# Performance work log

Measured on AMD Instinct MI355X. Metric: run time of the kernel, lower is better.

Reference implementation:

```python
import jax, jax.numpy as jnp
import numpy as np

R = 4e-4
NON = 0.05


def _conv1x1(x, w, b):
    # 1x1 conv, NCHW: [B,C,H,W] x [D,C] -> [B,D,H,W]
    return jnp.einsum('bchw,dc->bdhw', x, w) + b[None, :, None, None]


def _branch(x, si_w, si_b, fi_w, fi_b, gi_w, gi_b, fsg_w, fsg_b):
    B, C, W, H = x.shape
    N = W * H
    s = _conv1x1(x, si_w, si_b).reshape(B, C, N)
    f = _conv1x1(x, fi_w, fi_b).reshape(B, C, N)
    g = _conv1x1(x, gi_w, gi_b).reshape(B, C, N)
    # F = s^T @ f : [B, N, N]
    Fm = jnp.einsum('bcn,bcm->bnm', s, f)
    # original normalizes by global (per-sample) max & sum over the whole
    # [N,N] matrix -> a softmax over the flattened matrix. The exp-sum is
    # always > 0 (exp(0)=1 at the max), so the conditional is always taken.
    NF = jax.nn.softmax(Fm.reshape(B, N * N), axis=-1).reshape(B, N, N)
    gn = jnp.einsum('bcn,bnm->bcm', g, NF).reshape(B, C, W, H)
    fsg = _conv1x1(gn, fsg_w, fsg_b)
    # spatial mean pooling of residual sum -> [B, C]
    return (x + fsg).sum(axis=(2, 3)) / N


def setup_inputs() -> dict:
    key = jax.random.key(0)
    ks = jax.random.split(key, 10)
    B, C, W, H = 4, 64, 64, 64
    sc = 1.0 / np.sqrt(C)
    d = {
        'student': jax.random.normal(ks[0], (B, C, W, H), jnp.float32),
        'teacher': jax.random.normal(ks[1], (B, C, W, H), jnp.float32),
    }
    for i, nm in enumerate(['si', 'fi', 'gi', 'fsg']):
        d[nm + '_w'] = jax.random.normal(ks[2 + 2 * i], (C, C), jnp.float32) * sc
        d[nm + '_b'] = jax.random.normal(ks[3 + 2 * i], (C,), jnp.float32) * sc
    return d


def reference(student, teacher, si_w, si_b, fi_w, fi_b, gi_w, gi_b, fsg_w, fsg_b):
    out_stu = _branch(student, si_w, si_b, fi_w, fi_b, gi_w, gi_b, fsg_w, fsg_b)
    out_tea = _branch(teacher, si_w, si_b, fi_w, fi_b, gi_w, gi_b, fsg_w, fsg_b)
    B = student.shape[0]
    n_levels = 1  # len(student) in the original list-of-features API
    lnon = jnp.sum((out_stu - out_tea) ** 2)  # MSELoss(reduction='sum')
    non_loss = NON * R * lnon / B / n_levels
    return non_loss * B, jax.lax.stop_gradient(non_loss)[None]
```

## Files before the change

### kernel.cpp

```cpp
#include <hip/hip_runtime.h>
#include <hip/hip_bf16.h>
#include <stdint.h>

typedef __bf16 bf16x8 __attribute__((ext_vector_type(8)));
typedef float  f32x4  __attribute__((ext_vector_type(4)));

union U16x8 { bf16x8 v; unsigned short s[8]; uint4 q; };

#define SCH_SCALE 12102203.0f
#define SCH_BIAS  1064986823.0f

__device__ inline unsigned short f2bf(float f) {
  union { float f; unsigned int u; } x; x.f = f;
  unsigned int r = x.u + 0x7FFFu + ((x.u >> 16) & 1u);
  return (unsigned short)(r >> 16);
}
__device__ inline float bf2f(unsigned short u) {
  union { unsigned int u; float f; } x; x.u = ((unsigned int)u) << 16; return x.f;
}

__global__ __launch_bounds__(256) void k_proj(
    const float* __restrict__ stu, const float* __restrict__ tea,
    const float* __restrict__ si_w, const float* __restrict__ fi_w, const float* __restrict__ gi_w,
    const float* __restrict__ si_b, const float* __restrict__ fi_b, const float* __restrict__ gi_b,
    unsigned short* __restrict__ sT, unsigned short* __restrict__ fT, unsigned short* __restrict__ gT,
    float* __restrict__ Sxp) {
  int bid = blockIdx.x;
  int br_ba = bid & 7;
  int nt = bid >> 3;
  int br = br_ba >> 2, ba = br_ba & 3;
  const float* x = (br ? tea : stu) + (size_t)ba * 64 * 4096;
  int t = threadIdx.x;
  int wid = t >> 6, l = t & 63, g = l >> 4, lr = l & 15;
  int n0 = nt * 128 + wid * 32;

  U16x8 afr[2][2];
  float sx[2][8];
  #pragma unroll
  for (int kh = 0; kh < 2; ++kh)
    #pragma unroll
    for (int j = 0; j < 8; ++j) sx[kh][j] = 0.f;

  #pragma unroll
  for (int rf = 0; rf < 2; ++rf) {
    int n = n0 + rf * 16 + lr;
    #pragma unroll
    for (int kh = 0; kh < 2; ++kh) {
      #pragma unroll
      for (int j = 0; j < 8; ++j) {
        int c = kh * 32 + g * 8 + j;
        float v = x[(size_t)c * 4096 + n];
        afr[rf][kh].s[j] = f2bf(v);
        sx[kh][j] += v;
      }
    }
  }
  #pragma unroll
  for (int kh = 0; kh < 2; ++kh)
    #pragma unroll
    for (int j = 0; j < 8; ++j) {
      float v = sx[kh][j];
      v += __shfl_xor(v, 1); v += __shfl_xor(v, 2);
      v += __shfl_xor(v, 4); v += __shfl_xor(v, 8);
      sx[kh][j] = v;
    }
  __shared__ float sxl[4][64];
  if (lr == 0) {
    #pragma unroll
    for (int kh = 0; kh < 2; ++kh)
      #pragma unroll
      for (int j = 0; j < 8; ++j)
        sxl[wid][kh * 32 + g * 8 + j] = sx[kh][j];
  }
  __syncthreads();
  if (t < 64)
    Sxp[bid * 64 + t] = (sxl[0][t] + sxl[1][t]) + (sxl[2][t] + sxl[3][t]);

  size_t obase = (size_t)br_ba * 4096 * 64;
  auto proj_one = [&](const float* w, const float* bias, float scale,
                      unsigned short* op, int frag) {
    U16x8 bfr[4][2];
    #pragma unroll
    for (int cf = 0; cf < 4; ++cf) {
      int d = cf * 16 + lr;
      #pragma unroll
      for (int kh = 0; kh < 2; ++kh) {
        const float* wr = w + d * 64 + kh * 32 + g * 8;
        float4 w0 = *(const float4*)(wr);
        float4 w1 = *(const float4*)(wr + 4);
        bfr[cf][kh].s[0] = f2bf(w0.x * scale); bfr[cf][kh].s[1] = f2bf(w0.y * scale);
        bfr[cf][kh].s[2] = f2bf(w0.z * scale); bfr[cf][kh].s[3] = f2bf(w0.w * scale);
        bfr[cf][kh].s[4] = f2bf(w1.x * scale); bfr[cf][kh].s[5] = f2bf(w1.y * scale);
        bfr[cf][kh].s[6] = f2bf(w1.z * scale); bfr[cf][kh].s[7] = f2bf(w1.w * scale);
      }
    }
    f32x4 acc[2][4];
    #pragma unroll
    for (int rf = 0; rf < 2; ++rf)
      #pragma unroll
      for (int cf = 0; cf < 4; ++cf)
        acc[rf][cf] = (f32x4){0.f, 0.f, 0.f, 0.f};
    #pragma unroll
    for (int kh = 0; kh < 2; ++kh)
      #pragma unroll
      for (int rf = 0; rf < 2; ++rf)
        #pragma unroll
        for (int cf = 0; cf < 4; ++cf)
          acc[rf][cf] = __builtin_amdgcn_mfma_f32_16x16x32_bf16(
              afr[rf][kh].v, bfr[cf][kh].v, acc[rf][cf], 0, 0, 0);
    #pragma unroll
    for (int cf = 0; cf < 4; ++cf) {
      float bias_v = bias[cf * 16 + lr] * scale;
      int c = cf * 16 + lr;
      #pragma unroll
      for (int rf = 0; rf < 2; ++rf) {
        int sl = nt * 8 + wid * 2 + rf;
        #pragma unroll
        for (int r = 0; r < 4; ++r) {
          int n = n0 + rf * 16 + g * 4 + r;
          unsigned short val = f2bf(acc[rf][cf][r] + bias_v);
          if (frag) {
            size_t idx = ((size_t)(sl * 2 + (c >> 5)) * 64
                          + (g * 4 + r) + 16 * ((c >> 3) & 3)) * 8 + (c & 7);
            op[idx] = val;
          } else {
            op[(size_t)n * 64 + c] = val;
          }
        }
      }
    }
  };
  proj_one(si_w, si_b, SCH_SCALE, sT + obase, 1);
  proj_one(fi_w, fi_b, 1.0f, fT + obase, 1);
  proj_one(gi_w, gi_b, 1.0f, gT + obase, 0);
}

__global__ __launch_bounds__(256) void k_scores(
    const unsigned short* __restrict__ sT, const unsigned short* __restrict__ fT,
    float* __restrict__ stats_w) {
  int bid = blockIdx.x;
  int br_ba = bid & 7;
  int rest = bid >> 3;
  int cg = rest & 15;
  int rg = rest >> 4;
  int t = threadIdx.x;
  int wid = t >> 6, l = t & 63, g = l >> 4, lr = l & 15;

  const bf16x8* sfr = (const bf16x8*)sT + (size_t)br_ba * 32768;
  const bf16x8* ffr = (const bf16x8*)fT + (size_t)br_ba * 32768;

  const bf16x8* sp = sfr + (size_t)(cg * 16 + wid * 4) * 128 + l;
  bf16x8 b0k0 = sp[0];   bf16x8 b0k1 = sp[64];
  bf16x8 b1k0 = sp[128]; bf16x8 b1k1 = sp[192];
  bf16x8 b2k0 = sp[256]; bf16x8 b2k1 = sp[320];
  bf16x8 b3k0 = sp[384]; bf16x8 b3k1 = sp[448];

  const bf16x8* fp = ffr + (size_t)(rg * 32) * 128 + l;

  const f32x4 biasv = (f32x4){SCH_BIAS, SCH_BIAS, SCH_BIAS, SCH_BIAS};
  f32x4 S0 = (f32x4){0.f,0.f,0.f,0.f}, S1 = S0, S2 = S0, S3 = S0;

  bf16x8 cur0 = fp[0], cur1 = fp[64];

  #pragma unroll 2
  for (int k = 0; k < 32; ++k) {
    bf16x8 nxt0, nxt1;
    if (k < 31) {
      nxt0 = fp[(size_t)(k + 1) * 128];
      nxt1 = fp[(size_t)(k + 1) * 128 + 64];
    }
    f32x4 a0 = __builtin_amdgcn_mfma_f32_16x16x32_bf16(cur0, b0k0, biasv, 0,0,0);
    f32x4 a1 = __builtin_amdgcn_mfma_f32_16x16x32_bf16(cur0, b1k0, biasv, 0,0,0);
    f32x4 a2 = __builtin_amdgcn_mfma_f32_16x16x32_bf16(cur0, b2k0, biasv, 0,0,0);
    f32x4 a3 = __builtin_amdgcn_mfma_f32_16x16x32_bf16(cur0, b3k0, biasv, 0,0,0);
    a0 = __builtin_amdgcn_mfma_f32_16x16x32_bf16(cur1, b0k1, a0, 0,0,0);
    a1 = __builtin_amdgcn_mfma_f32_16x16x32_bf16(cur1, b1k1, a1, 0,0,0);
    a2 = __builtin_amdgcn_mfma_f32_16x16x32_bf16(cur1, b2k1, a2, 0,0,0);
    a3 = __builtin_amdgcn_mfma_f32_16x16x32_bf16(cur1, b3k1, a3, 0,0,0);
    #pragma unroll
    for (int r = 0; r < 4; ++r) {
      S0[r] += __uint_as_float((unsigned int)a0[r]);
      S1[r] += __uint_as_float((unsigned int)a1[r]);
      S2[r] += __uint_as_float((unsigned int)a2[r]);
      S3[r] += __uint_as_float((unsigned int)a3[r]);
    }
    cur0 = nxt0; cur1 = nxt1;
  }

  float w0 = (S0[0] + S0[1]) + (S0[2] + S0[3]);
  float w1 = (S1[0] + S1[1]) + (S1[2] + S1[3]);
  float w2 = (S2[0] + S2[1]) + (S2[2] + S2[3]);
  float w3 = (S3[0] + S3[1]) + (S3[2] + S3[3]);
  w0 += __shfl_xor(w0, 16); w0 += __shfl_xor(w0, 32);
  w1 += __shfl_xor(w1, 16); w1 += __shfl_xor(w1, 32);
  w2 += __shfl_xor(w2, 16); w2 += __shfl_xor(w2, 32);
  w3 += __shfl_xor(w3, 16); w3 += __shfl_xor(w3, 32);
  if (g == 0) {
    size_t cb = (size_t)br_ba * 4096 + cg * 256 + wid * 64 + lr;
    stats_w[(cb +  0) * 8 + rg] = w0;
    stats_w[(cb + 16) * 8 + rg] = w1;
    stats_w[(cb + 32) * 8 + rg] = w2;
    stats_w[(cb + 48) * 8 + rg] = w3;
  }
}

__global__ __launch_bounds__(256) void k_gbar(const unsigned short* __restrict__ gT,
                                              const float* __restrict__ stats_w,
                                              float* __restrict__ gbar_part,
                                              float* __restrict__ zpart) {
  int bid = blockIdx.x;
  int br_ba = bid & 7;
  int seg = bid >> 3;
  int t = threadIdx.x;
  int n0 = seg * 64;

  __shared__ float wlds[64];
  if (t < 64) {
    const float4* p = (const float4*)(stats_w + ((size_t)br_ba * 4096 + n0 + t) * 8);
    float4 a = p[0], b = p[1];
    float w = ((a.x + a.y) + (a.z + a.w)) + ((b.x + b.y) + (b.z + b.w));
    float zsum = w;
    zsum += __shfl_xor(zsum, 1);  zsum += __shfl_xor(zsum, 2);
    zsum += __shfl_xor(zsum, 4);  zsum += __shfl_xor(zsum, 8);
    zsum += __shfl_xor(zsum, 16); zsum += __shfl_xor(zsum, 32);
    if (t == 0) zpart[br_ba * 64 + seg] = zsum;
    wlds[t] = w;
  }
  __syncthreads();

  int c = t & 63, part = t >> 6;
  const unsigned short* gp = gT + ((size_t)br_ba * 4096 + n0) * 64;
  float acc = 0.f;
  #pragma unroll 4
  for (int r = 0; r < 16; ++r) {
    int k = part * 16 + r;
    acc += wlds[k] * bf2f(gp[(size_t)k * 64 + c]);
  }
  __shared__ float red[256];
  red[t] = acc; __syncthreads();
  if (t < 64)
    gbar_part[(size_t)(br_ba * 64 + seg) * 64 + c] =
        red[t] + red[t + 64] + red[t + 128] + red[t + 192];
}

__global__ __launch_bounds__(256) void k_loss(const float* __restrict__ Sxp,
                                              const float* __restrict__ gbar_part,
                                              const float* __restrict__ zpart,
                                              const float* __restrict__ fsg_w,
                                              float* __restrict__ out) {
  int t = threadIdx.x;
  int ba = t >> 6, d = t & 63;
  __shared__ float zsh[8];
  if (t < 8) {
    float z = 0.f;
    for (int s2 = 0; s2 < 64; ++s2) z += zpart[t * 64 + s2];
    zsh[t] = z;
  }
  float gs = 0.f, gt_ = 0.f;
  for (int seg = 0; seg < 64; ++seg) {
    gs  += gbar_part[(size_t)((0 + ba) * 64 + seg) * 64 + d];
    gt_ += gbar_part[(size_t)((4 + ba) * 64 + seg) * 64 + d];
  }
  float sxs = 0.f, sxt = 0.f;
  for (int nt = 0; nt < 32; ++nt) {
    sxs += Sxp[(nt * 8 + 0 + ba) * 64 + d];
    sxt += Sxp[(nt * 8 + 4 + ba) * 64 + d];
  }
  __syncthreads();
  __shared__ float gdiff[4][64];
  gdiff[ba][d] = gs / zsh[ba] - gt_ / zsh[4 + ba];
  __syncthreads();
  float dot = 0.f;
  for (int c = 0; c < 64; ++c) dot += fsg_w[d * 64 + c] * gdiff[ba][c];
  float diff = ((sxs - sxt) + dot) * (1.0f / 4096.0f);
  __shared__ float red[256];
  red[t] = diff * diff; __syncthreads();
  for (int s = 128; s > 0; s >>= 1) { if (t < s) red[t] += red[t + s]; __syncthreads(); }
  if (t == 0) {
    float lnon = red[0];
    out[0] = 2e-5f * lnon;
    out[1] = 2e-5f * lnon * 0.25f;
  }
}

extern "C" void kernel_launch(void* const* d_in, const int* in_sizes, int n_in,
                              void* d_out, int out_size, void* d_ws, size_t ws_size,
                              hipStream_t stream) {
  const float* stu   = (const float*)d_in[0];
  const float* tea   = (const float*)d_in[1];
  const float* si_w  = (const float*)d_in[2];
  const float* si_b  = (const float*)d_in[3];
  const float* fi_w  = (const float*)d_in[4];
  const float* fi_b  = (const float*)d_in[5];
  const float* gi_w  = (const float*)d_in[6];
  const float* gi_b  = (const float*)d_in[7];
  const float* fsg_w = (const float*)d_in[8];

  char* ws = (char*)d_ws;
  size_t off = 0;
  auto alloc = [&](size_t bytes) -> void* {
    void* p = ws + off;
    off = (off + bytes + 255) & ~(size_t)255;
    return p;
  };
  unsigned short* sT  = (unsigned short*)alloc((size_t)8 * 4096 * 64 * 2);
  unsigned short* fT  = (unsigned short*)alloc((size_t)8 * 4096 * 64 * 2);
  unsigned short* gT  = (unsigned short*)alloc((size_t)8 * 4096 * 64 * 2);
  float* stats_w      = (float*)alloc((size_t)8 * 4096 * 8 * 4);
  float* Sxp          = (float*)alloc((size_t)256 * 64 * 4);
  float* zpart        = (float*)alloc(512 * 4);
  float* gbar_part    = (float*)alloc((size_t)8 * 64 * 64 * 4);
  float* out          = (float*)d_out;

  k_proj<<<256, 256, 0, stream>>>(stu, tea, si_w, fi_w, gi_w, si_b, fi_b, gi_b, sT, fT, gT, Sxp);
  k_scores<<<1024, 256, 0, stream>>>(sT, fT, stats_w);
  k_gbar<<<512, 256, 0, stream>>>(gT, stats_w, gbar_part, zpart);
  k_loss<<<1, 256, 0, stream>>>(Sxp, gbar_part, zpart, fsg_w, out);
}
```

Measured before the change: 46.13 us.

## Fuse gbar and loss kernels via last-block atomic ticket reduction

Merges the gbar partial-sum kernel and the single-block loss kernel into one launch: each block atomically takes a ticket and the last block to finish does the final reduction and loss. The grid drops from 512 to 128 blocks, each covering 256 positions instead of 64, so there are fewer partials to reduce. The counter is zeroed inside k_proj. This removes one kernel launch and its gap, but lowers parallelism in the gbar phase and adds threadfence/atomic overhead.

Result: slower. 52.62 us (+14.1%).

```diff
diff --git a/kernel.cpp b/kernel.cpp
--- a/kernel.cpp
+++ b/kernel.cpp
@@ -24,8 +24,9 @@
     const float* __restrict__ si_w, const float* __restrict__ fi_w, const float* __restrict__ gi_w,
     const float* __restrict__ si_b, const float* __restrict__ fi_b, const float* __restrict__ gi_b,
     unsigned short* __restrict__ sT, unsigned short* __restrict__ fT, unsigned short* __restrict__ gT,
-    float* __restrict__ Sxp) {
+    float* __restrict__ Sxp, unsigned int* __restrict__ counter) {
   int bid = blockIdx.x;
+  if (bid == 0 && threadIdx.x == 0) *counter = 0;
   int br_ba = bid & 7;
   int nt = bid >> 3;
   int br = br_ba >> 2, ba = br_ba & 3;
@@ -204,64 +205,76 @@
   }
 }
 
-__global__ __launch_bounds__(256) void k_gbar(const unsigned short* __restrict__ gT,
-                                              const float* __restrict__ stats_w,
-                                              float* __restrict__ gbar_part,
-                                              float* __restrict__ zpart) {
+__global__ __launch_bounds__(256) void k_gbar_loss(
+    const unsigned short* __restrict__ gT,
+    const float* __restrict__ stats_w,
+    const float* __restrict__ Sxp,
+    const float* __restrict__ fsg_w,
+    float* __restrict__ gbar_part, float* __restrict__ zpart,
+    unsigned int* __restrict__ counter,
+    float* __restrict__ out) {
   int bid = blockIdx.x;
   int br_ba = bid & 7;
   int seg = bid >> 3;
   int t = threadIdx.x;
-  int n0 = seg * 64;
-
-  __shared__ float wlds[64];
-  if (t < 64) {
+  int n0 = seg * 256;
+
+  __shared__ float wlds[256];
+  {
     const float4* p = (const float4*)(stats_w + ((size_t)br_ba * 4096 + n0 + t) * 8);
     float4 a = p[0], b = p[1];
-    float w = ((a.x + a.y) + (a.z + a.w)) + ((b.x + b.y) + (b.z + b.w));
-    float zsum = w;
-    zsum += __shfl_xor(zsum, 1);  zsum += __shfl_xor(zsum, 2);
-    zsum += __shfl_xor(zsum, 4);  zsum += __shfl_xor(zsum, 8);
-    zsum += __shfl_xor(zsum, 16); zsum += __shfl_xor(zsum, 32);
-    if (t == 0) zpart[br_ba * 64 + seg] = zsum;
-    wlds[t] = w;
-  }
+    wlds[t] = ((a.x + a.y) + (a.z + a.w)) + ((b.x + b.y) + (b.z + b.w));
+  }
+  __syncthreads();
+
+  __shared__ float red[256];
+  red[t] = wlds[t]; __syncthreads();
+  for (int s = 128; s > 0; s >>= 1) { if (t < s) red[t] += red[t + s]; __syncthreads(); }
+  if (t == 0) zpart[bid] = red[0];
   __syncthreads();
 
   int c = t & 63, part = t >> 6;
   const unsigned short* gp = gT + ((size_t)br_ba * 4096 + n0) * 64;
   float acc = 0.f;
-  #pragma unroll 4
-  for (int r = 0; r < 16; ++r) {
-    int k = part * 16 + r;
+  #pragma unroll 8
+  for (int r = 0; r < 64; ++r) {
+    int k = part * 64 + r;
     acc += wlds[k] * bf2f(gp[(size_t)k * 64 + c]);
   }
-  __shared__ float red[256];
   red[t] = acc; __syncthreads();
   if (t < 64)
-    gbar_part[(size_t)(br_ba * 64 + seg) * 64 + c] =
+    gbar_part[(size_t)(br_ba * 16 + seg) * 64 + c] =
         red[t] + red[t + 64] + red[t + 128] + red[t + 192];
-}
-
-__global__ __launch_bounds__(256) void k_loss(const float* __restrict__ Sxp,
-                                              const float* __restrict__ gbar_part,
-                                              const float* __restrict__ zpart,
-                                              const float* __restrict__ fsg_w,
-                                              float* __restrict__ out) {
-  int t = threadIdx.x;
+
+  __threadfence();
+  __shared__ unsigned int ticket;
+  __syncthreads();
+  if (t == 0) ticket = atomicAdd(counter, 1u);
+  __syncthreads();
+  if (ticket != 127u) return;
+  __threadfence();
+
   int ba = t >> 6, d = t & 63;
   __shared__ float zsh[8];
+  if (t < 128) {
+    float zp = zpart[t];
+    red[t] = zp;
+  }
+  __syncthreads();
   if (t < 8) {
     float z = 0.f;
-    for (int s2 = 0; s2 < 64; ++s2) z += zpart[t * 64 + s2];
+    #pragma unroll
+    for (int s2 = 0; s2 < 16; ++s2) z += red[s2 * 8 + t];
     zsh[t] = z;
   }
   float gs = 0.f, gt_ = 0.f;
-  for (int seg = 0; seg < 64; ++seg) {
-    gs  += gbar_part[(size_t)((0 + ba) * 64 + seg) * 64 + d];
-    gt_ += gbar_part[(size_t)((4 + ba) * 64 + seg) * 64 + d];
+  #pragma unroll
+  for (int seg2 = 0; seg2 < 16; ++seg2) {
+    gs  += gbar_part[(size_t)((0 + ba) * 16 + seg2) * 64 + d];
+    gt_ += gbar_part[(size_t)((4 + ba) * 16 + seg2) * 64 + d];
   }
   float sxs = 0.f, sxt = 0.f;
+  #pragma unroll 8
   for (int nt = 0; nt < 32; ++nt) {
     sxs += Sxp[(nt * 8 + 0 + ba) * 64 + d];
     sxt += Sxp[(nt * 8 + 4 + ba) * 64 + d];
@@ -271,9 +284,9 @@
   gdiff[ba][d] = gs / zsh[ba] - gt_ / zsh[4 + ba];
   __syncthreads();
   float dot = 0.f;
-  for (int c = 0; c < 64; ++c) dot += fsg_w[d * 64 + c] * gdiff[ba][c];
+  #pragma unroll 8
+  for (int cc = 0; cc < 64; ++cc) dot += fsg_w[d * 64 + cc] * gdiff[ba][cc];
   float diff = ((sxs - sxt) + dot) * (1.0f / 4096.0f);
-  __shared__ float red[256];
   red[t] = diff * diff; __syncthreads();
   for (int s = 128; s > 0; s >>= 1) { if (t < s) red[t] += red[t + s]; __syncthreads(); }
   if (t == 0) {
@@ -308,12 +321,14 @@
   unsigned short* gT  = (unsigned short*)alloc((size_t)8 * 4096 * 64 * 2);
   float* stats_w      = (float*)alloc((size_t)8 * 4096 * 8 * 4);
   float* Sxp          = (float*)alloc((size_t)256 * 64 * 4);
-  float* zpart        = (float*)alloc(512 * 4);
-  float* gbar_part    = (float*)alloc((size_t)8 * 64 * 64 * 4);
+  float* zpart        = (float*)alloc(128 * 4);
+  float* gbar_part    = (float*)alloc((size_t)8 * 16 * 64 * 4);
+  unsigned int* cnt   = (unsigned int*)alloc(4);
   float* out          = (float*)d_out;
 
-  k_proj<<<256, 256, 0, stream>>>(stu, tea, si_w, fi_w, gi_w, si_b, fi_b, gi_b, sT, fT, gT, Sxp);
+  k_proj<<<256, 256, 0, stream>>>(stu, tea, si_w, fi_w, gi_w, si_b, fi_b, gi_b,
+                                  sT, fT, gT, Sxp, cnt);
   k_scores<<<1024, 256, 0, stream>>>(sT, fT, stats_w);
-  k_gbar<<<512, 256, 0, stream>>>(gT, stats_w, gbar_part, zpart);
-  k_loss<<<1, 256, 0, stream>>>(Sxp, gbar_part, zpart, fsg_w, out);
-}
+  k_gbar_loss<<<128, 256, 0, stream>>>(gT, stats_w, Sxp, fsg_w,
+                                       gbar_part, zpart, cnt, out);
+}
```
